# Optimization experiments

Hardware: AMD Instinct MI355X
Metric: run time of the kernel (lower is better)

## Reference

```python
import jax, jax.numpy as jnp
import numpy as np

N_QUBITS = 4
N_LAYERS = 2
DIM = 1 << N_QUBITS  # 16-dim state vector

# --- fixed (parameter-free) CNOT entangler layers, precomputed as 16x16 permutations ---

def _cnot_perm(c, t):
    M = np.zeros((DIM, DIM), np.complex64)
    for b in range(DIM):
        b2 = b ^ (1 << (N_QUBITS - 1 - t)) if (b >> (N_QUBITS - 1 - c)) & 1 else b
        M[b2, b] = 1.0
    return M

def _entangler(r):
    E = np.eye(DIM, dtype=np.complex64)
    for i in range(N_QUBITS):  # pennylane applies CNOT(i, (i+r)%n) sequentially
        E = _cnot_perm(i, (i + r) % N_QUBITS) @ E
    return E

ENT = [jnp.asarray(_entangler((l % (N_QUBITS - 1)) + 1)) for l in range(N_LAYERS)]
# Z_TABLE[b, w] = <b| Z_w |b>
Z_TABLE = jnp.asarray(np.array([[1.0 - 2.0 * ((b >> (N_QUBITS - 1 - w)) & 1) for w in range(N_QUBITS)] for b in range(DIM)], np.float32))


def _rot(phi, theta, omega):
    # pennylane Rot = RZ(omega) @ RY(theta) @ RZ(phi)
    c = jnp.cos(theta / 2).astype(jnp.complex64)
    s = jnp.sin(theta / 2).astype(jnp.complex64)
    a = jnp.exp(-0.5j * (phi + omega)) * c
    b = -jnp.exp(0.5j * (phi - omega)) * s
    cc = jnp.exp(-0.5j * (phi - omega)) * s
    d = jnp.exp(0.5j * (phi + omega)) * c
    return jnp.stack([jnp.stack([a, b]), jnp.stack([cc, d])])


def _vqc_unitary(weights):
    # weights: [N_LAYERS, N_QUBITS, 3] -> 16x16 unitary for StronglyEntanglingLayers
    U = jnp.eye(DIM, dtype=jnp.complex64)
    for l in range(N_LAYERS):
        R = _rot(weights[l, 0, 0], weights[l, 0, 1], weights[l, 0, 2])
        for q in range(1, N_QUBITS):  # wire 0 is most-significant bit -> left kron factor
            R = jnp.kron(R, _rot(weights[l, q, 0], weights[l, q, 1], weights[l, q, 2]))
        U = ENT[l] @ (R @ U)
    return U


def _vqc(x, weights):
    # x: [..., 4] rotation angles; AngleEmbedding uses RX: RX(a)|0> = [cos(a/2), -i sin(a/2)]
    c = jnp.cos(x / 2).astype(jnp.complex64)
    s = jnp.sin(x / 2).astype(jnp.complex64)
    amp = jnp.stack([c, -1j * s], axis=-1)  # [..., 4, 2]
    psi0 = jnp.einsum('...a,...b,...c,...d->...abcd', amp[..., 0, :], amp[..., 1, :], amp[..., 2, :], amp[..., 3, :])
    psi0 = psi0.reshape(x.shape[:-1] + (DIM,))
    U = _vqc_unitary(weights)
    psi = jnp.einsum('ij,...j->...i', U, psi0)
    probs = psi.real ** 2 + psi.imag ** 2
    return probs @ Z_TABLE  # [..., 4] PauliZ expectation values


def setup_inputs() -> dict:
    key = jax.random.key(0)
    k0, k1, k2, k3 = jax.random.split(key, 4)
    H = 768
    B, S = 8, 2048
    embeddings = jax.random.normal(k0, (B, S, H), dtype=jnp.float32)
    lim = 1.0 / np.sqrt(H)
    Wq = jax.random.normal(k1, (N_QUBITS, H), dtype=jnp.float32) * lim
    Wk = jax.random.normal(k2, (N_QUBITS, H), dtype=jnp.float32) * lim
    bq = jnp.zeros((N_QUBITS,), jnp.float32)
    bk = jnp.zeros((N_QUBITS,), jnp.float32)
    vqc_weights = jax.random.uniform(k3, (N_LAYERS, N_QUBITS, 3), dtype=jnp.float32) * (2.0 * np.pi)
    return {'embeddings': embeddings, 'Wq': Wq, 'bq': bq, 'Wk': Wk, 'bk': bk, 'vqc_weights': vqc_weights}


def reference(embeddings, Wq, bq, Wk, bk, vqc_weights):
    Q = jnp.einsum('bsh,qh->bsq', embeddings, Wq) + bq  # [B,S,4]
    K = jnp.einsum('bsh,qh->bsq', embeddings, Wk) + bk
    Qv = _vqc(Q, vqc_weights)  # [B,S,4]
    Kv = _vqc(K, vqc_weights)
    attn = jax.nn.softmax(jnp.einsum('bsq,btq->bst', Qv, Kv), axis=-1)  # [B,S,S]
    return jnp.einsum('bst,bth->bsh', attn, embeddings)
```

## Files before the change

### kernel.cpp

```cpp
#include <hip/hip_runtime.h>

#define NB 8
#define NS 2048
#define NH 768
#define NPOS (NB*NS)

typedef short short8 __attribute__((ext_vector_type(8)));
typedef float floatx4 __attribute__((ext_vector_type(4)));

__device__ __forceinline__ unsigned pack_bf16(unsigned b0, unsigned b1) {
  return __builtin_amdgcn_perm(b1, b0, 0x07060302u);
}

#define GLOAD_LDS16(gp, lp) __builtin_amdgcn_global_load_lds( \
  (const __attribute__((address_space(1))) unsigned int*)(gp), \
  (__attribute__((address_space(3))) unsigned int*)(lp), 16, 0, 0)

__global__ __launch_bounds__(384) void epre_kernel(
    const float* __restrict__ E, const float* __restrict__ wts,
    float* __restrict__ Vre, float* __restrict__ Vim,
    unsigned short* __restrict__ ET) {
  int tc = blockIdx.x, hb = blockIdx.y, b = blockIdx.z;
  int tid = threadIdx.x;

  if (tc == 0 && hb == 0 && b == 0 && tid < 16) {
    int j = tid;
    float ar[16], ai[16];
#pragma unroll
    for (int i = 0; i < 16; i++) { ar[i] = (i == j) ? 1.f : 0.f; ai[i] = 0.f; }
#pragma unroll
    for (int l = 0; l < 2; l++) {
#pragma unroll
      for (int q = 0; q < 4; q++) {
        float phi = wts[(l*4+q)*3+0];
        float th  = wts[(l*4+q)*3+1];
        float om  = wts[(l*4+q)*3+2];
        float ct = cosf(0.5f*th), st = sinf(0.5f*th);
        float sm = 0.5f*(phi+om), df = 0.5f*(phi-om);
        float cs = cosf(sm), ss = sinf(sm), cd = cosf(df), sd = sinf(df);
        float Ar =  cs*ct, Ai = -ss*ct;
        float Br = -cd*st, Bi = -sd*st;
        float Cr =  cd*st, Ci = -sd*st;
        float Dr =  cs*ct, Di =  ss*ct;
        int pb = 1 << (3-q);
#pragma unroll
        for (int b0 = 0; b0 < 16; b0++) {
          if (b0 & pb) continue;
          int b1 = b0 | pb;
          float xr = ar[b0], xi = ai[b0], yr = ar[b1], yi = ai[b1];
          ar[b0] = Ar*xr - Ai*xi + Br*yr - Bi*yi;
          ai[b0] = Ar*xi + Ai*xr + Br*yi + Bi*yr;
          ar[b1] = Cr*xr - Ci*xi + Dr*yr - Di*yi;
          ai[b1] = Cr*xi + Ci*xr + Dr*yi + Di*yr;
        }
      }
      const int r = (l == 0) ? 1 : 2;
#pragma unroll
      for (int i2 = 0; i2 < 4; i2++) {
        int cb = 1 << (3-i2);
        int tb = 1 << (3-((i2+r)&3));
#pragma unroll
        for (int b0 = 0; b0 < 16; b0++) {
          if ((b0 & cb) && !(b0 & tb)) {
            int b1 = b0 | tb;
            float tr = ar[b0], ti = ai[b0];
            ar[b0] = ar[b1]; ai[b0] = ai[b1];
            ar[b1] = tr;     ai[b1] = ti;
          }
        }
      }
    }
    int pc = __popc((unsigned)j) & 3;
#pragma unroll
    for (int i = 0; i < 16; i++) {
      float vr = ar[i], vi = ai[i], orr, oi;
      if      (pc == 0) { orr =  vr; oi =  vi; }
      else if (pc == 1) { orr =  vi; oi = -vr; }
      else if (pc == 2) { orr = -vr; oi = -vi; }
      else              { orr = -vi; oi =  vr; }
      Vre[i*16+j] = orr;
      Vim[i*16+j] = oi;
    }
  }

  size_t tbase = ((size_t)((b*4 + hb)*64 + tc)) * 12288;
  const float* Eb = E + (size_t)b*NS*NH + (size_t)tc*32*NH + hb*192;
#pragma unroll
  for (int u = 0; u < 2; u++) {
    int unit = tid + 384*u;
    int q2 = unit / 192, h2 = unit % 192;
    unsigned hi4[4], lo4[4];
#pragma unroll
    for (int jp = 0; jp < 4; jp++) {
      float ea = Eb[(size_t)(q2*8 + 2*jp    )*NH + h2];
      float eb = Eb[(size_t)(q2*8 + 2*jp + 1)*NH + h2];
      unsigned ba = __float_as_uint(ea), bb = __float_as_uint(eb);
      float la = ea - __uint_as_float(ba & 0xFFFF0000u);
      float lb = eb - __uint_as_float(bb & 0xFFFF0000u);
      hi4[jp] = pack_bf16(ba, bb);
      lo4[jp] = pack_bf16(__float_as_uint(la), __float_as_uint(lb));
    }
    int off = h2*32 + ((q2 ^ ((h2>>1)&3))*8);
    *(uint4*)&ET[tbase + off]        = make_uint4(hi4[0],hi4[1],hi4[2],hi4[3]);
    *(uint4*)&ET[tbase + 6144 + off] = make_uint4(lo4[0],lo4[1],lo4[2],lo4[3]);
  }
}

__global__ __launch_bounds__(256) void proj_vqc_kernel(
    const float* __restrict__ E, const float* __restrict__ Wq, const float* __restrict__ bq,
    const float* __restrict__ Wk, const float* __restrict__ bk,
    const float* __restrict__ Vre, const float* __restrict__ Vim,
    float* __restrict__ Qv, float* __restrict__ Kv) {
  __shared__ __align__(16) float WqL[768*4];
  __shared__ __align__(16) float WkL[768*4];
  __shared__ float Vsh[2][16*17];
  int tid = threadIdx.x;
  for (int idx = tid; idx < 768*4; idx += 256) {
    int e = idx >> 2, w = idx & 3;
    WqL[e*4+w] = Wq[w*768+e];
    WkL[e*4+w] = Wk[w*768+e];
  }
  if (tid < 256) {
    int i = tid >> 4, jj = tid & 15;
    Vsh[0][i*17+jj] = Vre[tid];
    Vsh[1][i*17+jj] = Vim[tid];
  }
  __syncthreads();
  float bqr0=bq[0], bqr1=bq[1], bqr2=bq[2], bqr3=bq[3];
  float bkr0=bk[0], bkr1=bk[1], bkr2=bk[2], bkr3=bk[3];
  int lane = tid & 63;
  int wid  = blockIdx.x*4 + (tid >> 6);
  int nw   = gridDim.x*4;
  int grp  = lane >> 4;
  int i    = lane & 15;
  for (int pos = wid; pos < NPOS; pos += nw) {
    const float* er = E + (size_t)pos*768;
    float pq[4] = {0.f,0.f,0.f,0.f};
    float pk[4] = {0.f,0.f,0.f,0.f};
#pragma unroll
    for (int k2 = 0; k2 < 3; k2++) {
      float4 ev = *(const float4*)(er + lane*4 + 256*k2);
#pragma unroll
      for (int jj = 0; jj < 4; jj++) {
        int e = lane*4 + 256*k2 + jj;
        float evs = (jj==0) ? ev.x : (jj==1) ? ev.y : (jj==2) ? ev.z : ev.w;
        float4 wq4 = *(const float4*)&WqL[e*4];
        float4 wk4 = *(const float4*)&WkL[e*4];
        pq[0] += evs*wq4.x; pq[1] += evs*wq4.y; pq[2] += evs*wq4.z; pq[3] += evs*wq4.w;
        pk[0] += evs*wk4.x; pk[1] += evs*wk4.y; pk[2] += evs*wk4.z; pk[3] += evs*wk4.w;
      }
    }
    float part[8];
#pragma unroll
    for (int w = 0; w < 8; w++) {
      float v = (w < 4) ? pq[w] : pk[w-4];
      v += __shfl_xor(v, 32); v += __shfl_xor(v, 16); v += __shfl_xor(v, 8);
      v += __shfl_xor(v, 4);  v += __shfl_xor(v, 2);  v += __shfl_xor(v, 1);
      part[w] = v;
    }
    if (grp < 2) {
      float a0,a1,a2,a3;
      if (grp == 0) { a0=part[0]+bqr0; a1=part[1]+bqr1; a2=part[2]+bqr2; a3=part[3]+bqr3; }
      else          { a0=part[4]+bkr0; a1=part[5]+bkr1; a2=part[6]+bkr2; a3=part[7]+bkr3; }
      float c0=cosf(0.5f*a0), s0=sinf(0.5f*a0);
      float c1=cosf(0.5f*a1), s1=sinf(0.5f*a1);
      float c2=cosf(0.5f*a2), s2=sinf(0.5f*a2);
      float c3=cosf(0.5f*a3), s3=sinf(0.5f*a3);
      float m[16];
#pragma unroll
      for (int j2 = 0; j2 < 16; j2++) {
        float f0 = (j2 & 8) ? s0 : c0;
        float f1 = (j2 & 4) ? s1 : c1;
        float f2 = (j2 & 2) ? s2 : c2;
        float f3 = (j2 & 1) ? s3 : c3;
        m[j2] = f0*f1*f2*f3;
      }
      float re = 0.f, im = 0.f;
#pragma unroll
      for (int j2 = 0; j2 < 16; j2++) {
        re += Vsh[0][i*17+j2]*m[j2];
        im += Vsh[1][i*17+j2]*m[j2];
      }
      float pr = re*re + im*im;
      float r0 = (i & 8) ? -pr : pr;
      float r1 = (i & 4) ? -pr : pr;
      float r2 = (i & 2) ? -pr : pr;
      float r3 = (i & 1) ? -pr : pr;
#pragma unroll
      for (int off = 8; off >= 1; off >>= 1) {
        r0 += __shfl_xor(r0, off);
        r1 += __shfl_xor(r1, off);
        r2 += __shfl_xor(r2, off);
        r3 += __shfl_xor(r3, off);
      }
      if (i == 0) {
        float* dst = (grp == 0 ? Qv : Kv) + (size_t)pos*4;
        dst[0]=r0; dst[1]=r1; dst[2]=r2; dst[3]=r3;
      }
    }
  }
}

#define TKC 32

__global__ __launch_bounds__(512, 4) void attn_kernel(
    const unsigned short* __restrict__ ET, const float* __restrict__ Qv,
    const float* __restrict__ Kv, float* __restrict__ out) {
  int sblk = blockIdx.x;
  int hblk = blockIdx.y;
  int b    = blockIdx.z;
  int tid  = threadIdx.x;
  int lane = tid & 63;
  int w    = tid >> 6;

  __shared__ __align__(16) unsigned short sA[8192];
  __shared__ __align__(16) unsigned short sB[2][12288];
  __shared__ float denp[128*4];
  __shared__ float dfin[128];

  const unsigned short* tE = ET + ((size_t)((b*4 + hblk)*64)) * 12288;
  const float* Kvb = Kv + (size_t)b*NS*4;

  int sP = tid & 127, qP = tid >> 7;
  float4 qv = *(const float4*)&Qv[((size_t)(b*NS + sblk*128) + sP)*4];
  float den_acc = 0.f;
  int offA = sP*32 + ((qP ^ ((sP>>1)&3))*8);

  int sh = w & 1, hh = w >> 1;
  floatx4 acc[4][3];
#pragma unroll
  for (int i = 0; i < 4; i++)
#pragma unroll
    for (int jt = 0; jt < 3; jt++) acc[i][jt] = floatx4{0.f,0.f,0.f,0.f};

  int m16 = lane & 15, q16 = lane >> 4;
  int cidx = (q16 ^ ((m16 >> 1) & 3)) * 8;
  int t16 = tid * 8;

  uint4 ph, pl;

  auto kvload = [&](int tb, float4* kvr) {
    const float* kvp = Kvb + (size_t)(tb + qP*8)*4;
#pragma unroll
    for (int j = 0; j < 8; j++) kvr[j] = *(const float4*)(kvp + j*4);
  };

  auto pcompute = [&](const float4* kvr) {
    unsigned hi4[4], lo4[4];
    float dsum = 0.f;
#pragma unroll
    for (int jp = 0; jp < 4; jp++) {
      float4 ka = kvr[2*jp];
      float4 kb = kvr[2*jp+1];
      float arga = qv.x*ka.x + qv.y*ka.y + qv.z*ka.z + qv.w*ka.w;
      float argb = qv.x*kb.x + qv.y*kb.y + qv.z*kb.z + qv.w*kb.w;
      float pa = __expf(arga), pb = __expf(argb);
      dsum += pa + pb;
      unsigned bpa = __float_as_uint(pa), bpb = __float_as_uint(pb);
      float lpa = pa - __uint_as_float(bpa & 0xFFFF0000u);
      float lpb = pb - __uint_as_float(bpb & 0xFFFF0000u);
      hi4[jp] = pack_bf16(bpa, bpb);
      lo4[jp] = pack_bf16(__float_as_uint(lpa), __float_as_uint(lpb));
    }
    den_acc += dsum;
    ph = make_uint4(hi4[0],hi4[1],hi4[2],hi4[3]);
    pl = make_uint4(lo4[0],lo4[1],lo4[2],lo4[3]);
  };

  auto do_mfma = [&](const unsigned short* sBc) {
    short8 ah[4], al[4];
#pragma unroll
    for (int i = 0; i < 4; i++) {
      int srow = sh*64 + i*16 + m16;
      ah[i] = __builtin_bit_cast(short8, *(const uint4*)&sA[srow*TKC + cidx]);
      al[i] = __builtin_bit_cast(short8, *(const uint4*)&sA[4096 + srow*TKC + cidx]);
    }
#pragma unroll
    for (int jt = 0; jt < 3; jt++) {
      int hrow = hh*48 + jt*16 + m16;
      short8 bh_ = __builtin_bit_cast(short8, *(const uint4*)&sBc[hrow*TKC + cidx]);
      short8 bl_ = __builtin_bit_cast(short8, *(const uint4*)&sBc[6144 + hrow*TKC + cidx]);
#pragma unroll
      for (int i = 0; i < 4; i++) {
        acc[i][jt] = __builtin_amdgcn_mfma_f32_16x16x32_bf16(ah[i], bl_, acc[i][jt], 0, 0, 0);
        acc[i][jt] = __builtin_amdgcn_mfma_f32_16x16x32_bf16(al[i], bh_, acc[i][jt], 0, 0, 0);
        acc[i][jt] = __builtin_amdgcn_mfma_f32_16x16x32_bf16(ah[i], bh_, acc[i][jt], 0, 0, 0);
      }
    }
  };

  {
    float4 kvr[8];
    kvload(0, kvr);
    GLOAD_LDS16(tE + t16,        &sB[0][0] + t16);
    GLOAD_LDS16(tE + 4096 + t16, &sB[0][0] + 4096 + t16);
    GLOAD_LDS16(tE + 8192 + t16, &sB[0][0] + 8192 + t16);
    pcompute(kvr);
  }

  for (int ci = 0; ci < 63; ci++) {
    int cb = ci & 1;

    __syncthreads();
    *(uint4*)&sA[offA]        = ph;
    *(uint4*)&sA[4096 + offA] = pl;
    __syncthreads();

    float4 kvr[8];
    kvload((ci+1)*TKC, kvr);

    const unsigned short* nE = tE + (size_t)(ci+1)*12288;
    unsigned short* sBn = &sB[cb^1][0];
    GLOAD_LDS16(nE + t16,        sBn + t16);
    GLOAD_LDS16(nE + 4096 + t16, sBn + 4096 + t16);
    GLOAD_LDS16(nE + 8192 + t16, sBn + 8192 + t16);

    pcompute(kvr);

    do_mfma(&sB[cb][0]);
  }

  __syncthreads();
  *(uint4*)&sA[offA]        = ph;
  *(uint4*)&sA[4096 + offA] = pl;
  __syncthreads();
  do_mfma(&sB[1][0]);

  denp[sP*4 + qP] = den_acc;
  __syncthreads();
  if (tid < 128) {
    dfin[tid] = denp[tid*4] + denp[tid*4+1] + denp[tid*4+2] + denp[tid*4+3];
  }
  __syncthreads();

  float* ob = out + ((size_t)(b*NS + sblk*128))*NH + hblk*192;
#pragma unroll
  for (int i = 0; i < 4; i++) {
#pragma unroll
    for (int reg = 0; reg < 4; reg++) {
      int row = q16*4 + reg;
      int s_loc = sh*64 + i*16 + row;
      float invd = 1.0f / dfin[s_loc];
#pragma unroll
      for (int jt = 0; jt < 3; jt++) {
        int h_loc = hh*48 + jt*16 + m16;
        ob[(size_t)s_loc*NH + h_loc] = acc[i][jt][reg] * invd;
      }
    }
  }
}

extern "C" void kernel_launch(void* const* d_in, const int* in_sizes, int n_in,
                              void* d_out, int out_size, void* d_ws, size_t ws_size,
                              hipStream_t stream) {
  const float* E   = (const float*)d_in[0];
  const float* Wq  = (const float*)d_in[1];
  const float* bq  = (const float*)d_in[2];
  const float* Wk  = (const float*)d_in[3];
  const float* bk  = (const float*)d_in[4];
  const float* wts = (const float*)d_in[5];
  float* ws  = (float*)d_ws;
  float* Vre = ws;
  float* Vim = ws + 256;
  float* Qv  = ws + 512;
  float* Kv  = Qv + (size_t)NPOS*4;
  unsigned short* ET = (unsigned short*)(Kv + (size_t)NPOS*4);
  float* out = (float*)d_out;

  epre_kernel<<<dim3(64, 4, 8), 384, 0, stream>>>(E, wts, Vre, Vim, ET);
  proj_vqc_kernel<<<1024, 256, 0, stream>>>(E, Wq, bq, Wk, bk, Vre, Vim, Qv, Kv);
  attn_kernel<<<dim3(16, 4, 8), 512, 0, stream>>>(ET, Qv, Kv, out);
}
```

Baseline: 286.4 us.

## Switch split-bf16 MFMA to fp16 with single-precision P and double-buffered sA

Result: faster. 258.8 us (-9.6%).

```diff
diff --git a/kernel.cpp b/kernel.cpp
--- a/kernel.cpp
+++ b/kernel.cpp
@@ -5,12 +5,8 @@
 #define NH 768
 #define NPOS (NB*NS)
 
-typedef short short8 __attribute__((ext_vector_type(8)));
+typedef _Float16 half8 __attribute__((ext_vector_type(8)));
 typedef float floatx4 __attribute__((ext_vector_type(4)));
-
-__device__ __forceinline__ unsigned pack_bf16(unsigned b0, unsigned b1) {
-  return __builtin_amdgcn_perm(b1, b0, 0x07060302u);
-}
 
 #define GLOAD_LDS16(gp, lp) __builtin_amdgcn_global_load_lds( \
   (const __attribute__((address_space(1))) unsigned int*)(gp), \
@@ -94,11 +90,14 @@
     for (int jp = 0; jp < 4; jp++) {
       float ea = Eb[(size_t)(q2*8 + 2*jp    )*NH + h2];
       float eb = Eb[(size_t)(q2*8 + 2*jp + 1)*NH + h2];
-      unsigned ba = __float_as_uint(ea), bb = __float_as_uint(eb);
-      float la = ea - __uint_as_float(ba & 0xFFFF0000u);
-      float lb = eb - __uint_as_float(bb & 0xFFFF0000u);
-      hi4[jp] = pack_bf16(ba, bb);
-      lo4[jp] = pack_bf16(__float_as_uint(la), __float_as_uint(lb));
+      _Float16 ha = (_Float16)ea, hb16 = (_Float16)eb;
+      float la = ea - (float)ha, lb = eb - (float)hb16;
+      unsigned uha = __builtin_bit_cast(unsigned short, ha);
+      unsigned uhb = __builtin_bit_cast(unsigned short, hb16);
+      unsigned ula = __builtin_bit_cast(unsigned short, (_Float16)la);
+      unsigned ulb = __builtin_bit_cast(unsigned short, (_Float16)lb);
+      hi4[jp] = uha | (uhb << 16);
+      lo4[jp] = ula | (ulb << 16);
     }
     int off = h2*32 + ((q2 ^ ((h2>>1)&3))*8);
     *(uint4*)&ET[tbase + off]        = make_uint4(hi4[0],hi4[1],hi4[2],hi4[3]);
@@ -213,7 +212,7 @@
   int lane = tid & 63;
   int w    = tid >> 6;
 
-  __shared__ __align__(16) unsigned short sA[8192];
+  __shared__ __align__(16) unsigned short sA[2][4096];
   __shared__ __align__(16) unsigned short sB[2][12288];
   __shared__ float denp[128*4];
   __shared__ float dfin[128];
@@ -237,16 +236,14 @@
   int cidx = (q16 ^ ((m16 >> 1) & 3)) * 8;
   int t16 = tid * 8;
 
-  uint4 ph, pl;
-
   auto kvload = [&](int tb, float4* kvr) {
     const float* kvp = Kvb + (size_t)(tb + qP*8)*4;
 #pragma unroll
     for (int j = 0; j < 8; j++) kvr[j] = *(const float4*)(kvp + j*4);
   };
 
-  auto pcompute = [&](const float4* kvr) {
-    unsigned hi4[4], lo4[4];
+  auto pcompute = [&](const float4* kvr) -> uint4 {
+    unsigned h4[4];
     float dsum = 0.f;
 #pragma unroll
     for (int jp = 0; jp < 4; jp++) {
@@ -256,35 +253,30 @@
       float argb = qv.x*kb.x + qv.y*kb.y + qv.z*kb.z + qv.w*kb.w;
       float pa = __expf(arga), pb = __expf(argb);
       dsum += pa + pb;
-      unsigned bpa = __float_as_uint(pa), bpb = __float_as_uint(pb);
-      float lpa = pa - __uint_as_float(bpa & 0xFFFF0000u);
-      float lpb = pb - __uint_as_float(bpb & 0xFFFF0000u);
-      hi4[jp] = pack_bf16(bpa, bpb);
-      lo4[jp] = pack_bf16(__float_as_uint(lpa), __float_as_uint(lpb));
+      unsigned ua = (unsigned)__builtin_bit_cast(unsigned short, (_Float16)pa);
+      unsigned ub = (unsigned)__builtin_bit_cast(unsigned short, (_Float16)pb);
+      h4[jp] = ua | (ub << 16);
     }
     den_acc += dsum;
-    ph = make_uint4(hi4[0],hi4[1],hi4[2],hi4[3]);
-    pl = make_uint4(lo4[0],lo4[1],lo4[2],lo4[3]);
+    return make_uint4(h4[0], h4[1], h4[2], h4[3]);
   };
 
-  auto do_mfma = [&](const unsigned short* sBc) {
-    short8 ah[4], al[4];
+  auto do_mfma = [&](const unsigned short* sAc, const unsigned short* sBc) {
+    half8 a[4];
 #pragma unroll
     for (int i = 0; i < 4; i++) {
       int srow = sh*64 + i*16 + m16;
-      ah[i] = __builtin_bit_cast(short8, *(const uint4*)&sA[srow*TKC + cidx]);
-      al[i] = __builtin_bit_cast(short8, *(const uint4*)&sA[4096 + srow*TKC + cidx]);
+      a[i] = __builtin_bit_cast(half8, *(const uint4*)&sAc[srow*TKC + cidx]);
     }
 #pragma unroll
     for (int jt = 0; jt < 3; jt++) {
       int hrow = hh*48 + jt*16 + m16;
-      short8 bh_ = __builtin_bit_cast(short8, *(const uint4*)&sBc[hrow*TKC + cidx]);
-      short8 bl_ = __builtin_bit_cast(short8, *(const uint4*)&sBc[6144 + hrow*TKC + cidx]);
+      half8 bh_ = __builtin_bit_cast(half8, *(const uint4*)&sBc[hrow*TKC + cidx]);
+      half8 bl_ = __builtin_bit_cast(half8, *(const uint4*)&sBc[6144 + hrow*TKC + cidx]);
 #pragma unroll
       for (int i = 0; i < 4; i++) {
-        acc[i][jt] = __builtin_amdgcn_mfma_f32_16x16x32_bf16(ah[i], bl_, acc[i][jt], 0, 0, 0);
-        acc[i][jt] = __builtin_amdgcn_mfma_f32_16x16x32_bf16(al[i], bh_, acc[i][jt], 0, 0, 0);
-        acc[i][jt] = __builtin_amdgcn_mfma_f32_16x16x32_bf16(ah[i], bh_, acc[i][jt], 0, 0, 0);
+        acc[i][jt] = __builtin_amdgcn_mfma_f32_16x16x32_f16(a[i], bl_, acc[i][jt], 0, 0, 0);
+        acc[i][jt] = __builtin_amdgcn_mfma_f32_16x16x32_f16(a[i], bh_, acc[i][jt], 0, 0, 0);
       }
     }
   };
@@ -295,37 +287,28 @@
     GLOAD_LDS16(tE + t16,        &sB[0][0] + t16);
     GLOAD_LDS16(tE + 4096 + t16, &sB[0][0] + 4096 + t16);
     GLOAD_LDS16(tE + 8192 + t16, &sB[0][0] + 8192 + t16);
-    pcompute(kvr);
-  }
-
-  for (int ci = 0; ci < 63; ci++) {
+    uint4 ph = pcompute(kvr);
+    *(uint4*)&sA[0][offA] = ph;
+  }
+
+  for (int ci = 0; ci < 64; ci++) {
     int cb = ci & 1;
-
     __syncthreads();
-    *(uint4*)&sA[offA]        = ph;
-    *(uint4*)&sA[4096 + offA] = pl;
-    __syncthreads();
-
-    float4 kvr[8];
-    kvload((ci+1)*TKC, kvr);
-
-    const unsigned short* nE = tE + (size_t)(ci+1)*12288;
-    unsigned short* sBn = &sB[cb^1][0];
-    GLOAD_LDS16(nE + t16,        sBn + t16);
-    GLOAD_LDS16(nE + 4096 + t16, sBn + 4096 + t16);
-    GLOAD_LDS16(nE + 8192 + t16, sBn + 8192 + t16);
-
-    pcompute(kvr);
-
-    do_mfma(&sB[cb][0]);
+    if (ci < 63) {
+      float4 kvr[8];
+      kvload((ci+1)*TKC, kvr);
+      const unsigned short* nE = tE + (size_t)(ci+1)*12288;
+      unsigned short* sBn = &sB[cb^1][0];
+      GLOAD_LDS16(nE + t16,        sBn + t16);
+      GLOAD_LDS16(nE + 4096 + t16, sBn + 4096 + t16);
+      GLOAD_LDS16(nE + 8192 + t16, sBn + 8192 + t16);
+      uint4 ph = pcompute(kvr);
+      *(uint4*)&sA[cb^1][offA] = ph;
+    }
+    do_mfma(&sA[cb][0], &sB[cb][0]);
   }
 
   __syncthreads();
-  *(uint4*)&sA[offA]        = ph;
-  *(uint4*)&sA[4096 + offA] = pl;
-  __syncthreads();
-  do_mfma(&sB[1][0]);
-
   denp[sP*4 + qP] = den_acc;
   __syncthreads();
   if (tid < 128) {
```
